# Optimization experiments

Hardware: AMD Instinct MI355X
Metric: run time of the kernel (lower is better)

Reference implementation:

```python
import jax, jax.numpy as jnp
import numpy as np

D = 1024      # d_model
ED = 2048     # d_inner
K = 4         # d_conv
N = 16        # d_state
R = 64        # dt_rank
E = 8         # num_experts
TOPK = 2      # num_experts_per_tok
FF = 2048     # mlp_size
EPS = 1e-6
B, L = 1, 2048


def setup_inputs() -> dict:
    key = jax.random.key(0)
    ks = jax.random.split(key, 12)
    def nrm(k, shape, scale=0.02):
        return jax.random.normal(k, shape, jnp.float32) * scale
    return {
        "x": jax.random.normal(ks[0], (B, L, D), jnp.float32),
        "rms1_w": jnp.ones((D,), jnp.float32),
        "rms2_w": jnp.ones((D,), jnp.float32),
        "W_in": nrm(ks[1], (2 * ED, D)),
        "conv_w": nrm(ks[2], (ED, 1, K), 0.1),
        "conv_b": jnp.zeros((ED,), jnp.float32),
        "W_xproj": nrm(ks[3], (R + 2 * N, ED)),
        "W_dt": nrm(ks[4], (ED, R), 0.1),
        "b_dt": jnp.full((ED,), -4.6, jnp.float32),  # softplus(-4.6) ~ 0.01 init dt
        "A_log": jnp.log(jnp.tile(jnp.arange(1, N + 1, dtype=jnp.float32), (ED, 1))),  # S4D-real init
        "D_skip": jnp.ones((ED,), jnp.float32),
        "W_out": nrm(ks[5], (D, ED)),
        "W_router": nrm(ks[6], (E, D)),
        "gate_w": nrm(ks[7], (E, FF, D)),
        "up_w": nrm(ks[8], (E, FF, D)),
        "down_w": nrm(ks[9], (E, D, FF)),
    }


def rmsnorm(x, w):
    return x * jax.lax.rsqrt(jnp.mean(x * x, -1, keepdims=True) + EPS) * w


def mamba(x, W_in, conv_w, conv_b, W_xproj, W_dt, b_dt, A_log, D_skip, W_out):
    Bb, Ll, _ = x.shape
    xm, z = jnp.split(x @ W_in.T, 2, axis=-1)                 # [B,L,ED] each
    # depthwise causal conv over time
    xc = jax.lax.conv_general_dilated(xm.transpose(0, 2, 1), conv_w, (1,), [(K - 1, 0)],
                                      feature_group_count=ED)  # [B,ED,L]
    xc = jax.nn.silu((xc + conv_b[None, :, None]).transpose(0, 2, 1))  # [B,L,ED]
    dt, Bm, Cm = jnp.split(xc @ W_xproj.T, [R, R + N], axis=-1)        # [B,L,R],[B,L,N],[B,L,N]
    delta = jax.nn.softplus(dt @ W_dt.T + b_dt)                        # [B,L,ED]
    A = -jnp.exp(A_log)                                                # [ED,N]
    dA = jnp.exp(delta[..., None] * A)                                 # [B,L,ED,N]
    dBx = delta[..., None] * Bm[:, :, None, :] * xc[..., None]         # [B,L,ED,N]

    def step(h, t):
        dA_t, dBx_t, C_t = t
        h = dA_t * h + dBx_t
        return h, jnp.einsum("ben,bn->be", h, C_t)

    h0 = jnp.zeros((Bb, ED, N), x.dtype)
    _, ys = jax.lax.scan(step, h0, (dA.transpose(1, 0, 2, 3), dBx.transpose(1, 0, 2, 3), Cm.transpose(1, 0, 2)))
    y = ys.transpose(1, 0, 2) + D_skip * xc
    y = y * jax.nn.silu(z)
    return y @ W_out.T


def moe(x2d, W_router, gate_w, up_w, down_w):
    logits = x2d @ W_router.T                                  # [T,E]
    probs = jax.nn.softmax(logits.astype(jnp.float32), -1)
    topw, sel = jax.lax.top_k(probs, TOPK)                     # NOTE: no renormalization (faithful)
    topw = topw.astype(x2d.dtype)
    wmat = jnp.sum(jax.nn.one_hot(sel, E, dtype=x2d.dtype) * topw[..., None], axis=1)  # [T,E]
    g = jnp.einsum("td,efd->tef", x2d, gate_w)
    u = jnp.einsum("td,efd->tef", x2d, up_w)
    h = jax.nn.silu(g) * u
    ye = jnp.einsum("tef,edf->ted", h, down_w)
    out = jnp.einsum("ted,te->td", ye, wmat)
    return out, logits


def reference(x, rms1_w, rms2_w, W_in, conv_w, conv_b, W_xproj, W_dt, b_dt, A_log,
              D_skip, W_out, W_router, gate_w, up_w, down_w):
    Bb, Ll, Dd = x.shape
    res = x
    h = rmsnorm(x, rms1_w)
    h = mamba(h, W_in, conv_w, conv_b, W_xproj, W_dt, b_dt, A_log, D_skip, W_out)
    x = res + h
    res = x
    h = rmsnorm(x, rms2_w)
    mo, logits = moe(h.reshape(-1, Dd), W_router, gate_w, up_w, down_w)
    x = res + mo.reshape(Bb, Ll, Dd)
    return (x, logits)
```

## Files before the change

kernel.cpp:

```cpp
#include <hip/hip_runtime.h>
#include <math.h>

typedef unsigned short u16;
typedef unsigned int   u32;
typedef __attribute__((ext_vector_type(8))) short bf16x8;
typedef __attribute__((ext_vector_type(4))) float f32x4;

constexpr int Tn=2048, Dm=1024, EDc=2048, Ns=16, Rr=64, NEx=8, FFc=2048;
constexpr int SCH=32, SNCH=Tn/SCH;
constexpr int MAXTM=40;
constexpr float LOG2E = 1.44269504f;

__device__ __forceinline__ float siluf(float x){ return __fdividef(x, 1.f + __expf(-x)); }
__device__ __forceinline__ u16 bfr(float f){
  u32 u = __float_as_uint(f);
  return (u16)((u + 0x7fffu + ((u>>16)&1u)) >> 16);
}
__device__ __forceinline__ float b2f(u16 h){ return __uint_as_float(((u32)h)<<16); }

__device__ __forceinline__ void gload16(const void* g, void* l){
  __builtin_amdgcn_global_load_lds((const __attribute__((address_space(1))) void*)g,
                                   (__attribute__((address_space(3))) void*)l, 16, 0, 0);
}

__global__ __launch_bounds__(256) void f2b_k(const float* __restrict__ in,
                                             u16* __restrict__ out, int n4){
  int i = blockIdx.x*256 + threadIdx.x;
  if (i >= n4) return;
  float4 v = ((const float4*)in)[i];
  u32 lo = (u32)bfr(v.x) | ((u32)bfr(v.y)<<16);
  u32 hi = (u32)bfr(v.z) | ((u32)bfr(v.w)<<16);
  ((uint2*)out)[i] = make_uint2(lo, hi);
}

__global__ __launch_bounds__(256) void f2b3_k(
    const float* __restrict__ g, const float* __restrict__ u,
    const float* __restrict__ d,
    u16* __restrict__ og, u16* __restrict__ ou, u16* __restrict__ od){
  const int BPW = (NEx*FFc*Dm/4)/256;
  int b = blockIdx.x;
  int which = b / BPW;
  int i = (b - which*BPW)*256 + threadIdx.x;
  const float* in = (which==0) ? g : (which==1) ? u : d;
  u16* out        = (which==0) ? og : (which==1) ? ou : od;
  float4 v = ((const float4*)in)[i];
  u32 lo = (u32)bfr(v.x) | ((u32)bfr(v.y)<<16);
  u32 hi = (u32)bfr(v.z) | ((u32)bfr(v.w)<<16);
  ((uint2*)out)[i] = make_uint2(lo, hi);
}

__global__ __launch_bounds__(256) void rmsnorm_k(const float* __restrict__ x,
                                                 const float* __restrict__ w,
                                                 u16* __restrict__ ob){
  int t = blockIdx.x;
  const float* xr = x + (size_t)t * Dm;
  float v[4]; float s = 0.f;
#pragma unroll
  for (int j = 0; j < 4; j++){ int d = threadIdx.x + j*256; v[j] = xr[d]; s += v[j]*v[j]; }
#pragma unroll
  for (int m = 1; m < 64; m <<= 1) s += __shfl_xor(s, m);
  __shared__ float red[4]; __shared__ float sb;
  int lane = threadIdx.x & 63, wv = threadIdx.x >> 6;
  if (lane == 0) red[wv] = s;
  __syncthreads();
  if (threadIdx.x == 0) sb = rsqrtf((red[0]+red[1]+red[2]+red[3]) * (1.f/Dm) + 1e-6f);
  __syncthreads();
  float sc = sb;
#pragma unroll
  for (int j = 0; j < 4; j++){
    int d = threadIdx.x + j*256;
    ob[(size_t)t*Dm + d] = bfr(v[j]*sc*w[d]);
  }
}

__global__ __launch_bounds__(256) void rms2red_k(
  const float* __restrict__ x, const float* __restrict__ P,
  const float* __restrict__ w,
  float* __restrict__ out, float* __restrict__ h2f, u16* __restrict__ h2b)
{
  int t = blockIdx.x, tid = threadIdx.x;
  const size_t S = (size_t)Tn*Dm;
  float v[4]; float s = 0.f;
#pragma unroll
  for (int j = 0; j < 4; j++){
    int d = tid + j*256;
    size_t idx = (size_t)t*Dm + d;
    float a = x[idx] + ((P[idx] + P[S+idx]) + (P[2*S+idx] + P[3*S+idx]));
    out[idx] = a; v[j] = a; s += a*a;
  }
#pragma unroll
  for (int m = 1; m < 64; m <<= 1) s += __shfl_xor(s, m);
  __shared__ float red[4]; __shared__ float sb;
  int lane = tid & 63, wv = tid >> 6;
  if (lane == 0) red[wv] = s;
  __syncthreads();
  if (tid == 0) sb = rsqrtf((red[0]+red[1]+red[2]+red[3]) * (1.f/Dm) + 1e-6f);
  __syncthreads();
  float sc = sb;
#pragma unroll
  for (int j = 0; j < 4; j++){
    int d = tid + j*256;
    float o = v[j]*sc*w[d];
    h2b[(size_t)t*Dm + d] = bfr(o);
    h2f[(size_t)t*Dm + d] = o;
  }
}

template<int EPI, int OB>
__global__ __launch_bounds__(512) void gemm_bb(
    const u16* __restrict__ A, int lda,
    const u16* __restrict__ B, int ldb,
    void* __restrict__ Cv, int ldc,
    int M, int N, int Ksl, const float* __restrict__ aux)
{
  __shared__ u16 As[2*4096], Bs[2*4096];
  int tid = threadIdx.x, lane = tid & 63, wid = tid >> 6;
  int wr = wid >> 2, wc = wid & 3;
  int n0 = blockIdx.x * 128, m0 = blockIdx.y * 128;
  int r = tid >> 2;
  int kk = ((tid & 3) ^ (r & 3)) * 8;
  size_t kbeg = (size_t)blockIdx.z * Ksl;
  const u16* Ag = A + (size_t)min(m0 + r, M-1)*lda + kbeg + kk;
  const u16* Bg = B + (size_t)min(n0 + r, N-1)*ldb + kbeg + kk;
  f32x4 acc[4][2] = {};
  int sw = ((lane>>4) ^ (lane&3)) * 8;
  int aoff[4], boff[2];
#pragma unroll
  for (int i = 0; i < 4; i++) aoff[i] = (wr*64 + i*16 + (lane&15))*32 + sw;
#pragma unroll
  for (int j = 0; j < 2; j++) boff[j] = (wc*32 + j*16 + (lane&15))*32 + sw;
  gload16(Ag, As + tid*8);
  gload16(Bg, Bs + tid*8);
  int NT = Ksl >> 5;
  for (int kt = 0; kt < NT; kt++){
    int cur = (kt & 1) * 4096;
    if (kt + 1 < NT){
      int nxt = 4096 - cur;
      gload16(Ag + (size_t)(kt+1)*32, As + nxt + tid*8);
      gload16(Bg + (size_t)(kt+1)*32, Bs + nxt + tid*8);
      asm volatile("s_waitcnt vmcnt(2)" ::: "memory");
    } else {
      asm volatile("s_waitcnt vmcnt(0)" ::: "memory");
    }
    __builtin_amdgcn_s_barrier();
    bf16x8 af[4], bv[2];
#pragma unroll
    for (int i = 0; i < 4; i++) af[i] = *(const bf16x8*)&As[cur + aoff[i]];
#pragma unroll
    for (int j = 0; j < 2; j++) bv[j] = *(const bf16x8*)&Bs[cur + boff[j]];
    asm volatile("s_waitcnt lgkmcnt(0)" ::: "memory");
    __builtin_amdgcn_sched_barrier(0);
    __builtin_amdgcn_s_barrier();
    __builtin_amdgcn_s_setprio(1);
#pragma unroll
    for (int i = 0; i < 4; i++)
#pragma unroll
      for (int j = 0; j < 2; j++)
        acc[i][j] = __builtin_amdgcn_mfma_f32_16x16x32_bf16(af[i], bv[j], acc[i][j], 0,0,0);
    __builtin_amdgcn_s_setprio(0);
  }
  float* Cf = (float*)Cv + (size_t)blockIdx.z * M * ldc;
  u16*   Cb = (u16*)Cv;
#pragma unroll
  for (int i = 0; i < 4; i++){
    int rbase = m0 + wr*64 + i*16 + ((lane>>4)<<2);
#pragma unroll
    for (int j = 0; j < 2; j++){
      int col = n0 + wc*32 + j*16 + (lane&15);
      if (col >= N) continue;
#pragma unroll
      for (int q = 0; q < 4; q++){
        int row = rbase + q;
        if (row >= M) continue;
        float v = acc[i][j][q];
        if (EPI == 1){ v += aux[col]; v = (v > 20.f) ? v : __logf(1.f + __expf(v)); }
        if (OB) Cb[(size_t)row*ldc + col] = bfr(v);
        else    Cf[(size_t)row*ldc + col] = v;
      }
    }
  }
}

__global__ __launch_bounds__(512) void gateup8(
    const u16* __restrict__ Aall,
    const u16* __restrict__ Wg, const u16* __restrict__ Wu,
    const int* __restrict__ cnt, const int* __restrict__ off,
    const int* __restrict__ bucket,
    const int* __restrict__ tmap, const int* __restrict__ ntot,
    u16* __restrict__ H)
{
  if ((int)blockIdx.y >= *ntot) return;
  int v = tmap[blockIdx.y];
  int e = v >> 16, m0 = (v & 0xFFFF) * 128;
  int Me = cnt[e];
  __shared__ u16 As[2*4096], Gs[2*4096], Us[2*4096];
  int tid = threadIdx.x, lane = tid & 63, wid = tid >> 6;
  int wr = wid >> 2, wc = wid & 3;
  int n0 = blockIdx.x * 128;
  int r = tid >> 2;
  int kk = ((tid & 3) ^ (r & 3)) * 8;
  int arow = bucket[e*Tn + min(m0 + r, Me-1)];
  const u16* Ag = Aall + (size_t)arow*Dm + kk;
  const u16* Gg = Wg + ((size_t)e*FFc + n0 + r)*Dm + kk;
  const u16* Ug = Wu + ((size_t)e*FFc + n0 + r)*Dm + kk;
  f32x4 ag[4][2] = {}, au[4][2] = {};
  int sw = ((lane>>4) ^ (lane&3)) * 8;
  int aoff[4], boff[2];
#pragma unroll
  for (int i = 0; i < 4; i++) aoff[i] = (wr*64 + i*16 + (lane&15))*32 + sw;
#pragma unroll
  for (int j = 0; j < 2; j++) boff[j] = (wc*32 + j*16 + (lane&15))*32 + sw;
  gload16(Ag, As + tid*8);
  gload16(Gg, Gs + tid*8);
  gload16(Ug, Us + tid*8);
  const int NT = Dm >> 5;
  for (int kt = 0; kt < NT; kt++){
    int cur = (kt & 1) * 4096;
    if (kt + 1 < NT){
      int nxt = 4096 - cur;
      gload16(Ag + (size_t)(kt+1)*32, As + nxt + tid*8);
      gload16(Gg + (size_t)(kt+1)*32, Gs + nxt + tid*8);
      gload16(Ug + (size_t)(kt+1)*32, Us + nxt + tid*8);
      asm volatile("s_waitcnt vmcnt(3)" ::: "memory");
    } else {
      asm volatile("s_waitcnt vmcnt(0)" ::: "memory");
    }
    __builtin_amdgcn_s_barrier();
    bf16x8 af[4], gf[2], uf[2];
#pragma unroll
    for (int i = 0; i < 4; i++) af[i] = *(const bf16x8*)&As[cur + aoff[i]];
#pragma unroll
    for (int j = 0; j < 2; j++){ gf[j] = *(const bf16x8*)&Gs[cur + boff[j]];
                                 uf[j] = *(const bf16x8*)&Us[cur + boff[j]]; }
    asm volatile("s_waitcnt lgkmcnt(0)" ::: "memory");
    __builtin_amdgcn_sched_barrier(0);
    __builtin_amdgcn_s_barrier();
    __builtin_amdgcn_s_setprio(1);
#pragma unroll
    for (int i = 0; i < 4; i++)
#pragma unroll
      for (int j = 0; j < 2; j++){
        ag[i][j] = __builtin_amdgcn_mfma_f32_16x16x32_bf16(af[i], gf[j], ag[i][j], 0,0,0);
        au[i][j] = __builtin_amdgcn_mfma_f32_16x16x32_bf16(af[i], uf[j], au[i][j], 0,0,0);
      }
    __builtin_amdgcn_s_setprio(0);
  }
  int offe = off[e];
#pragma unroll
  for (int i = 0; i < 4; i++){
    int mb = m0 + wr*64 + i*16 + ((lane>>4)<<2);
#pragma unroll
    for (int j = 0; j < 2; j++){
      int col = n0 + wc*32 + j*16 + (lane&15);
#pragma unroll
      for (int q = 0; q < 4; q++){
        int m = mb + q;
        if (m >= Me) continue;
        float g = ag[i][j][q], u = au[i][j][q];
        H[(size_t)(offe + m)*FFc + col] = bfr(siluf(g)*u);
      }
    }
  }
}

__global__ __launch_bounds__(512) void down8(
    const u16* __restrict__ Hall, const u16* __restrict__ Wd,
    const int* __restrict__ cnt, const int* __restrict__ off,
    const int* __restrict__ tmap, const int* __restrict__ ntot,
    u16* __restrict__ Y)
{
  if ((int)blockIdx.y >= *ntot) return;
  int v = tmap[blockIdx.y];
  int e = v >> 16, m0 = (v & 0xFFFF) * 128;
  int Me = cnt[e];
  int offe = off[e];
  int kbeg = blockIdx.z * (FFc/2);
  const u16* A = Hall + (size_t)offe*FFc;
  const u16* B = Wd + (size_t)e*Dm*FFc;
  u16* C = Y + (size_t)blockIdx.z*(2*Tn)*Dm + (size_t)offe*Dm;
  __shared__ u16 As[2*4096], Bs[2*4096];
  int tid = threadIdx.x, lane = tid & 63, wid = tid >> 6;
  int wr = wid >> 2, wc = wid & 3;
  int n0 = blockIdx.x * 128;
  int r = tid >> 2;
  int kk = ((tid & 3) ^ (r & 3)) * 8;
  const u16* Ag = A + (size_t)min(m0 + r, Me-1)*FFc + kbeg + kk;
  const u16* Bg = B + (size_t)(n0 + r)*FFc + kbeg + kk;
  f32x4 acc[4][2] = {};
  int sw = ((lane>>4) ^ (lane&3)) * 8;
  int aoff[4], boff[2];
#pragma unroll
  for (int i = 0; i < 4; i++) aoff[i] = (wr*64 + i*16 + (lane&15))*32 + sw;
#pragma unroll
  for (int j = 0; j < 2; j++) boff[j] = (wc*32 + j*16 + (lane&15))*32 + sw;
  gload16(Ag, As + tid*8);
  gload16(Bg, Bs + tid*8);
  const int NT = (FFc/2) >> 5;
  for (int kt = 0; kt < NT; kt++){
    int cur = (kt & 1) * 4096;
    if (kt + 1 < NT){
      int nxt = 4096 - cur;
      gload16(Ag + (size_t)(kt+1)*32, As + nxt + tid*8);
      gload16(Bg + (size_t)(kt+1)*32, Bs + nxt + tid*8);
      asm volatile("s_waitcnt vmcnt(2)" ::: "memory");
    } else {
      asm volatile("s_waitcnt vmcnt(0)" ::: "memory");
    }
    __builtin_amdgcn_s_barrier();
    bf16x8 af[4], bv[2];
#pragma unroll
    for (int i = 0; i < 4; i++) af[i] = *(const bf16x8*)&As[cur + aoff[i]];
#pragma unroll
    for (int j = 0; j < 2; j++) bv[j] = *(const bf16x8*)&Bs[cur + boff[j]];
    asm volatile("s_waitcnt lgkmcnt(0)" ::: "memory");
    __builtin_amdgcn_sched_barrier(0);
    __builtin_amdgcn_s_barrier();
    __builtin_amdgcn_s_setprio(1);
#pragma unroll
    for (int i = 0; i < 4; i++)
#pragma unroll
      for (int j = 0; j < 2; j++)
        acc[i][j] = __builtin_amdgcn_mfma_f32_16x16x32_bf16(af[i], bv[j], acc[i][j], 0,0,0);
    __builtin_amdgcn_s_setprio(0);
  }
#pragma unroll
  for (int i = 0; i < 4; i++){
    int mb = m0 + wr*64 + i*16 + ((lane>>4)<<2);
#pragma unroll
    for (int j = 0; j < 2; j++){
      int col = n0 + wc*32 + j*16 + (lane&15);
#pragma unroll
      for (int q = 0; q < 4; q++){
        int m = mb + q;
        if (m >= Me) continue;
        C[(size_t)m*Dm + col] = bfr(acc[i][j][q]);
      }
    }
  }
}

__global__ __launch_bounds__(256) void conv_k(const u16* __restrict__ xzb,
    const float* __restrict__ cw, const float* __restrict__ cb,
    u16* __restrict__ xc)
{
  int idx = blockIdx.x*256 + threadIdx.x;
  int t = idx >> 11, e = idx & (EDc - 1);
  float v = cb[e];
#pragma unroll
  for (int k = 0; k < 4; k++){
    int tt = t - 3 + k;
    if (tt >= 0) v += b2f(xzb[(size_t)tt*(2*EDc) + e]) * cw[e*4 + k];
  }
  xc[(size_t)t*EDc + e] = bfr(siluf(v));
}

__global__ __launch_bounds__(256) void xp_red(const float* __restrict__ part,
                                              float* __restrict__ xp,
                                              u16* __restrict__ dtA){
  int i = blockIdx.x*256 + threadIdx.x;
  const int S = Tn*96;
  float v = part[i] + part[S + i] + part[2*S + i] + part[3*S + i];
  xp[i] = v;
  int t = i / 96, c = i - t*96;
  if (c < Rr) dtA[t*Rr + c] = bfr(v);
}

__global__ __launch_bounds__(256) void scan_p1(
  const u16* __restrict__ delta, const u16* __restrict__ xc,
// ... 164 lines not shown
  __shared__ float lg[8];
  int lane = tid & 63, wv = tid >> 6;
  if (lane == 0)
#pragma unroll
    for (int e = 0; e < 8; e++) part[wv][e] = p[e];
  __syncthreads();
  if (tid < 8){
    float v = part[0][tid]+part[1][tid]+part[2][tid]+part[3][tid];
    lg[tid] = v;
    logits_out[(size_t)t*8 + tid] = v;
  }
  __syncthreads();
  if (tid == 0){
    float mx = lg[0];
#pragma unroll
    for (int e = 1; e < 8; e++) mx = fmaxf(mx, lg[e]);
    float ex[8], s = 0.f;
#pragma unroll
    for (int e = 0; e < 8; e++){ ex[e] = expf(lg[e] - mx); s += ex[e]; }
    float inv = 1.f / s;
    int i0 = 0; float b0 = ex[0]*inv;
#pragma unroll
    for (int e = 1; e < 8; e++){ float pe = ex[e]*inv; if (pe > b0){ b0 = pe; i0 = e; } }
    int i1 = -1; float b1 = -1e30f;
#pragma unroll
    for (int e = 0; e < 8; e++){ if (e == i0) continue; float pe = ex[e]*inv; if (pe > b1){ b1 = pe; i1 = e; } }
    int k0 = atomicAdd(&cnt[i0], 1); bucket[i0*Tn + k0] = t;
    int k1 = atomicAdd(&cnt[i1], 1); bucket[i1*Tn + k1] = t;
    tok_e[2*t] = i0;   tok_idx[2*t] = k0;   tok_w[2*t] = b0;
    tok_e[2*t+1] = i1; tok_idx[2*t+1] = k1; tok_w[2*t+1] = b1;
  }
}

__global__ void prefix_k(const int* __restrict__ cnt, int* __restrict__ off,
                         int* __restrict__ tmap, int* __restrict__ ntot){
  if (threadIdx.x == 0 && blockIdx.x == 0){
    int s = 0;
    for (int e = 0; e < NEx; e++){ off[e] = s; s += cnt[e]; }
    int nt = 0;
    for (int e = 0; e < NEx; e++){
      int tiles = (cnt[e] + 127) >> 7;
      for (int tm = 0; tm < tiles; tm++) tmap[nt++] = (e << 16) | tm;
    }
    *ntot = nt;
  }
}

__global__ __launch_bounds__(256) void combine_k(float* __restrict__ out,
    const u16* __restrict__ Y, const int* __restrict__ off,
    const int* __restrict__ tok_e, const int* __restrict__ tok_idx,
    const float* __restrict__ tok_w)
{
  int t = blockIdx.x, tid = threadIdx.x;
  const size_t S2 = (size_t)(2*Tn)*Dm;
  int e0 = tok_e[2*t],   e1 = tok_e[2*t+1];
  size_t r0 = (size_t)(off[e0] + tok_idx[2*t])*Dm;
  size_t r1 = (size_t)(off[e1] + tok_idx[2*t+1])*Dm;
  float w0 = tok_w[2*t], w1 = tok_w[2*t+1];
#pragma unroll
  for (int j = 0; j < 4; j++){
    int d = tid + j*256;
    float y0 = b2f(Y[r0 + d]) + b2f(Y[S2 + r0 + d]);
    float y1 = b2f(Y[r1 + d]) + b2f(Y[S2 + r1 + d]);
    out[(size_t)t*Dm + d] += w0*y0 + w1*y1;
  }
}

extern "C" void kernel_launch(void* const* d_in, const int* in_sizes, int n_in,
                              void* d_out, int out_size, void* d_ws, size_t ws_size,
                              hipStream_t stream) {
  const float* x      = (const float*)d_in[0];
  const float* rms1_w = (const float*)d_in[1];
  const float* rms2_w = (const float*)d_in[2];
  const float* W_in   = (const float*)d_in[3];
  const float* conv_w = (const float*)d_in[4];
  const float* conv_b = (const float*)d_in[5];
  const float* W_xprj = (const float*)d_in[6];
  const float* W_dt   = (const float*)d_in[7];
  const float* b_dt   = (const float*)d_in[8];
  const float* A_log  = (const float*)d_in[9];
  const float* D_skip = (const float*)d_in[10];
  const float* W_out  = (const float*)d_in[11];
  const float* W_rt   = (const float*)d_in[12];
  const float* gate_w = (const float*)d_in[13];
  const float* up_w   = (const float*)d_in[14];
  const float* down_w = (const float*)d_in[15];

  float* out        = (float*)d_out;
  float* logits_out = out + (size_t)Tn*Dm;

  uint8_t* base = (uint8_t*)d_ws;
  size_t o = 0;
  auto alloc = [&](size_t bytes) -> void* {
    void* p = base + o;
    o = (o + bytes + 255) & ~(size_t)255;
    return p;
  };
  float* h2f   = (float*)alloc((size_t)Tn*Dm*4);
  u16*   h2b   = (u16*)  alloc((size_t)Tn*Dm*2);
  u16*   hmoe  = (u16*)  alloc((size_t)2*Tn*FFc*2);
  u16*   yslot = (u16*)  alloc((size_t)2*(2*Tn)*Dm*2);
  int*   cnt     = (int*)alloc(64);
  int*   off     = (int*)alloc(64);
  int*   ntot    = (int*)alloc(64);
  int*   tmap    = (int*)alloc(MAXTM*4 + 192);
  int*   bucket  = (int*)alloc((size_t)NEx*Tn*4);
  int*   tok_e   = (int*)alloc((size_t)2*Tn*4);
  int*   tok_idx = (int*)alloc((size_t)2*Tn*4);
  float* tok_w   = (float*)alloc((size_t)2*Tn*4);
  size_t oz = o;
  u16*   xzb   = (u16*)  alloc((size_t)Tn*2*EDc*2);
  u16*   delta = (u16*)  alloc((size_t)Tn*EDc*2);
  u16*   xc    = (u16*)  alloc((size_t)Tn*EDc*2);
  u16*   y2    = (u16*)  alloc((size_t)Tn*EDc*2);
  u16*   h1b   = (u16*)  alloc((size_t)Tn*Dm*2);
  u16*   dtA   = (u16*)  alloc((size_t)Tn*Rr*2);
  float* xp    = (float*)alloc((size_t)Tn*96*4);
  float* xp_part=(float*)alloc((size_t)4*Tn*96*4);
  float* hend  = (float*)alloc((size_t)SNCH*EDc*Ns*4);
  float* hin   = (float*)alloc((size_t)SNCH*EDc*Ns*4);
  float* dsum  = (float*)alloc((size_t)SNCH*EDc*4);
  float* wpart = (float*)xzb;
  u16* wgate = (u16*)(base + oz);
  u16* wup   = wgate + (size_t)NEx*FFc*Dm;
  u16* wdown = wup   + (size_t)NEx*FFc*Dm;
  u16* wbin  = (u16*)yslot;
  u16* wbout = wbin + (size_t)2*EDc*Dm;
  u16* wxp   = (u16*)hmoe;
  u16* wdt   = wxp + (size_t)96*EDc;

  f2b_k<<<(2*EDc*Dm/4)/256, 256, 0, stream>>>(W_in,   wbin,  2*EDc*Dm/4);
  f2b_k<<<(Dm*EDc/4)/256,   256, 0, stream>>>(W_out,  wbout, Dm*EDc/4);
  f2b_k<<<(96*EDc/4)/256,   256, 0, stream>>>(W_xprj, wxp,   96*EDc/4);
  f2b_k<<<(EDc*Rr/4)/256,   256, 0, stream>>>(W_dt,   wdt,   EDc*Rr/4);
  rmsnorm_k<<<Tn, 256, 0, stream>>>(x, rms1_w, h1b);
  gemm_bb<0,1><<<dim3(32,16,1), 512, 0, stream>>>(h1b, Dm, wbin, Dm, xzb, 2*EDc, Tn, 2*EDc, Dm, nullptr);
  conv_k<<<(Tn*EDc)/256, 256, 0, stream>>>(xzb, conv_w, conv_b, xc);
  gemm_bb<0,0><<<dim3(1,16,4), 512, 0, stream>>>(xc, EDc, wxp, EDc, xp_part, 96, Tn, 96, EDc/4, nullptr);
  xp_red<<<(Tn*96)/256, 256, 0, stream>>>(xp_part, xp, dtA);
  gemm_bb<1,1><<<dim3(16,16,1), 512, 0, stream>>>(dtA, Rr, wdt, Rr, delta, EDc, Tn, EDc, Rr, b_dt);
  scan_p1<<<dim3(EDc/256, SNCH), 256, 0, stream>>>(delta, xc, xp, A_log, hend, dsum);
  scan_p2<<<EDc*Ns/256, 256, 0, stream>>>(hend, dsum, A_log, hin);
  scan_p3<<<dim3(EDc/256, SNCH), 256, 0, stream>>>(delta, xc, xp, xzb, A_log, D_skip, hin, y2);
  gemm_bb<0,0><<<dim3(8,16,4), 512, 0, stream>>>(y2, EDc, wbout, EDc, wpart, Dm, Tn, Dm, EDc/4, nullptr);
  rms2red_k<<<Tn, 256, 0, stream>>>(x, wpart, rms2_w, out, h2f, h2b);
  f2b3_k<<<3*((NEx*FFc*Dm/4)/256), 256, 0, stream>>>(gate_w, up_w, down_w, wgate, wup, wdown);
  hipMemsetAsync(cnt, 0, 32, stream);
  route_k<<<Tn, 256, 0, stream>>>(h2f, W_rt, logits_out, cnt, bucket, tok_e, tok_idx, tok_w);
  prefix_k<<<1, 64, 0, stream>>>(cnt, off, tmap, ntot);
  gateup8<<<dim3(16, MAXTM), 512, 0, stream>>>(h2b, wgate, wup, cnt, off, bucket, tmap, ntot, hmoe);
  down8<<<dim3(8, MAXTM, 2), 512, 0, stream>>>(hmoe, wdown, cnt, off, tmap, ntot, yslot);
  combine_k<<<Tn, 256, 0, stream>>>(out, yslot, off, tok_e, tok_idx, tok_w);
}
```

Baseline: 395.7 us.

## Fuse fp32-to-bf16 weight conversion into GEMM and MoE B-operand loads

Removes the separate passes that convert W_in, W_out and the expert gate, up and down weights to bf16. The GEMM and MoE kernels now read fp32 weights straight into registers, pack them with v_cvt_pk_bf16_f32 and store them to LDS, with the next tile's loads issued before the current MFMAs. This saves a full write and re-read of about 200MB of expert weights. In exchange the MoE GEMMs read twice as many weight bytes, repeated per token tile, and lose the async direct-to-LDS load path for B. The gate and up MFMA phases are also split so the up-weight LDS reads are issued separately.

```diff
diff --git a/kernel.cpp b/kernel.cpp
--- a/kernel.cpp
+++ b/kernel.cpp
@@ -17,6 +17,13 @@
   return (u16)((u + 0x7fffu + ((u>>16)&1u)) >> 16);
 }
 __device__ __forceinline__ float b2f(u16 h){ return __uint_as_float(((u32)h)<<16); }
+
+__device__ __forceinline__ u32 cvtpk(float lo, float hi){
+  u32 r; asm("v_cvt_pk_bf16_f32 %0, %1, %2" : "=v"(r) : "v"(lo), "v"(hi)); return r;
+}
+__device__ __forceinline__ uint4 cvt8(float4 a, float4 b){
+  return make_uint4(cvtpk(a.x,a.y), cvtpk(a.z,a.w), cvtpk(b.x,b.y), cvtpk(b.z,b.w));
+}
 
 __device__ __forceinline__ void gload16(const void* g, void* l){
   __builtin_amdgcn_global_load_lds((const __attribute__((address_space(1))) void*)g,
@@ -33,22 +40,6 @@
   ((uint2*)out)[i] = make_uint2(lo, hi);
 }
 
-__global__ __launch_bounds__(256) void f2b3_k(
-    const float* __restrict__ g, const float* __restrict__ u,
-    const float* __restrict__ d,
-    u16* __restrict__ og, u16* __restrict__ ou, u16* __restrict__ od){
-  const int BPW = (NEx*FFc*Dm/4)/256;
-  int b = blockIdx.x;
-  int which = b / BPW;
-  int i = (b - which*BPW)*256 + threadIdx.x;
-  const float* in = (which==0) ? g : (which==1) ? u : d;
-  u16* out        = (which==0) ? og : (which==1) ? ou : od;
-  float4 v = ((const float4*)in)[i];
-  u32 lo = (u32)bfr(v.x) | ((u32)bfr(v.y)<<16);
-  u32 hi = (u32)bfr(v.z) | ((u32)bfr(v.w)<<16);
-  ((uint2*)out)[i] = make_uint2(lo, hi);
-}
-
 __global__ __launch_bounds__(256) void rmsnorm_k(const float* __restrict__ x,
                                                  const float* __restrict__ w,
                                                  u16* __restrict__ ob){
@@ -106,10 +97,10 @@
   }
 }
 
-template<int EPI, int OB>
+template<int EPI, int OB, int BF32>
 __global__ __launch_bounds__(512) void gemm_bb(
     const u16* __restrict__ A, int lda,
-    const u16* __restrict__ B, int ldb,
+    const void* __restrict__ Bvp, int ldb,
     void* __restrict__ Cv, int ldc,
     int M, int N, int Ksl, const float* __restrict__ aux)
 {
@@ -121,7 +112,6 @@
   int kk = ((tid & 3) ^ (r & 3)) * 8;
   size_t kbeg = (size_t)blockIdx.z * Ksl;
   const u16* Ag = A + (size_t)min(m0 + r, M-1)*lda + kbeg + kk;
-  const u16* Bg = B + (size_t)min(n0 + r, N-1)*ldb + kbeg + kk;
   f32x4 acc[4][2] = {};
   int sw = ((lane>>4) ^ (lane&3)) * 8;
   int aoff[4], boff[2];
@@ -129,36 +119,81 @@
   for (int i = 0; i < 4; i++) aoff[i] = (wr*64 + i*16 + (lane&15))*32 + sw;
 #pragma unroll
   for (int j = 0; j < 2; j++) boff[j] = (wc*32 + j*16 + (lane&15))*32 + sw;
-  gload16(Ag, As + tid*8);
-  gload16(Bg, Bs + tid*8);
   int NT = Ksl >> 5;
-  for (int kt = 0; kt < NT; kt++){
-    int cur = (kt & 1) * 4096;
-    if (kt + 1 < NT){
-      int nxt = 4096 - cur;
-      gload16(Ag + (size_t)(kt+1)*32, As + nxt + tid*8);
-      gload16(Bg + (size_t)(kt+1)*32, Bs + nxt + tid*8);
-      asm volatile("s_waitcnt vmcnt(2)" ::: "memory");
-    } else {
+
+  if (BF32){
+    const float* Bg = (const float*)Bvp + (size_t)min(n0 + r, N-1)*ldb + kbeg + kk;
+    {
+      float4 q0 = *(const float4*)Bg;
+      float4 q1 = *(const float4*)(Bg + 4);
+      gload16(Ag, As + tid*8);
       asm volatile("s_waitcnt vmcnt(0)" ::: "memory");
-    }
-    __builtin_amdgcn_s_barrier();
-    bf16x8 af[4], bv[2];
-#pragma unroll
-    for (int i = 0; i < 4; i++) af[i] = *(const bf16x8*)&As[cur + aoff[i]];
-#pragma unroll
-    for (int j = 0; j < 2; j++) bv[j] = *(const bf16x8*)&Bs[cur + boff[j]];
-    asm volatile("s_waitcnt lgkmcnt(0)" ::: "memory");
-    __builtin_amdgcn_sched_barrier(0);
-    __builtin_amdgcn_s_barrier();
-    __builtin_amdgcn_s_setprio(1);
-#pragma unroll
-    for (int i = 0; i < 4; i++)
-#pragma unroll
-      for (int j = 0; j < 2; j++)
-        acc[i][j] = __builtin_amdgcn_mfma_f32_16x16x32_bf16(af[i], bv[j], acc[i][j], 0,0,0);
-    __builtin_amdgcn_s_setprio(0);
-  }
+      *(uint4*)&Bs[tid*8] = cvt8(q0, q1);
+    }
+    for (int kt = 0; kt < NT; kt++){
+      int cur = (kt & 1) * 4096, nxt = 4096 - cur;
+      bool pf = (kt + 1 < NT);
+      float4 p0{}, p1{};
+      if (pf){
+        p0 = *(const float4*)(Bg + (size_t)(kt+1)*32);
+        p1 = *(const float4*)(Bg + (size_t)(kt+1)*32 + 4);
+        gload16(Ag + (size_t)(kt+1)*32, As + nxt + tid*8);
+      }
+      asm volatile("s_waitcnt lgkmcnt(0)" ::: "memory");
+      __builtin_amdgcn_s_barrier();
+      bf16x8 af[4], bv[2];
+#pragma unroll
+      for (int i = 0; i < 4; i++) af[i] = *(const bf16x8*)&As[cur + aoff[i]];
+#pragma unroll
+      for (int j = 0; j < 2; j++) bv[j] = *(const bf16x8*)&Bs[cur + boff[j]];
+      asm volatile("s_waitcnt lgkmcnt(0)" ::: "memory");
+      __builtin_amdgcn_sched_barrier(0);
+      __builtin_amdgcn_s_barrier();
+      __builtin_amdgcn_s_setprio(1);
+#pragma unroll
+      for (int i = 0; i < 4; i++)
+#pragma unroll
+        for (int j = 0; j < 2; j++)
+          acc[i][j] = __builtin_amdgcn_mfma_f32_16x16x32_bf16(af[i], bv[j], acc[i][j], 0,0,0);
+      __builtin_amdgcn_s_setprio(0);
+      if (pf){
+        asm volatile("s_waitcnt vmcnt(0)" ::: "memory");
+        *(uint4*)&Bs[nxt + tid*8] = cvt8(p0, p1);
+      }
+    }
+  } else {
+    const u16* Bg = (const u16*)Bvp + (size_t)min(n0 + r, N-1)*ldb + kbeg + kk;
+    gload16(Ag, As + tid*8);
+    gload16(Bg, Bs + tid*8);
+    for (int kt = 0; kt < NT; kt++){
+      int cur = (kt & 1) * 4096;
+      if (kt + 1 < NT){
+        int nxt = 4096 - cur;
+        gload16(Ag + (size_t)(kt+1)*32, As + nxt + tid*8);
+        gload16(Bg + (size_t)(kt+1)*32, Bs + nxt + tid*8);
+        asm volatile("s_waitcnt vmcnt(2)" ::: "memory");
+      } else {
+        asm volatile("s_waitcnt vmcnt(0)" ::: "memory");
+      }
+      __builtin_amdgcn_s_barrier();
+      bf16x8 af[4], bv[2];
+#pragma unroll
+      for (int i = 0; i < 4; i++) af[i] = *(const bf16x8*)&As[cur + aoff[i]];
+#pragma unroll
+      for (int j = 0; j < 2; j++) bv[j] = *(const bf16x8*)&Bs[cur + boff[j]];
+      asm volatile("s_waitcnt lgkmcnt(0)" ::: "memory");
+      __builtin_amdgcn_sched_barrier(0);
+      __builtin_amdgcn_s_barrier();
+      __builtin_amdgcn_s_setprio(1);
+#pragma unroll
+      for (int i = 0; i < 4; i++)
+#pragma unroll
+        for (int j = 0; j < 2; j++)
+          acc[i][j] = __builtin_amdgcn_mfma_f32_16x16x32_bf16(af[i], bv[j], acc[i][j], 0,0,0);
+      __builtin_amdgcn_s_setprio(0);
+    }
+  }
+
   float* Cf = (float*)Cv + (size_t)blockIdx.z * M * ldc;
   u16*   Cb = (u16*)Cv;
 #pragma unroll
@@ -183,7 +218,7 @@
 
 __global__ __launch_bounds__(512) void gateup8(
     const u16* __restrict__ Aall,
-    const u16* __restrict__ Wg, const u16* __restrict__ Wu,
+    const float* __restrict__ Wg, const float* __restrict__ Wu,
     const int* __restrict__ cnt, const int* __restrict__ off,
     const int* __restrict__ bucket,
     const int* __restrict__ tmap, const int* __restrict__ ntot,
@@ -201,8 +236,8 @@
   int kk = ((tid & 3) ^ (r & 3)) * 8;
   int arow = bucket[e*Tn + min(m0 + r, Me-1)];
   const u16* Ag = Aall + (size_t)arow*Dm + kk;
-  const u16* Gg = Wg + ((size_t)e*FFc + n0 + r)*Dm + kk;
-  const u16* Ug = Wu + ((size_t)e*FFc + n0 + r)*Dm + kk;
+  const float* Gg = Wg + ((size_t)e*FFc + n0 + r)*Dm + kk;
+  const float* Ug = Wu + ((size_t)e*FFc + n0 + r)*Dm + kk;
   f32x4 ag[4][2] = {}, au[4][2] = {};
   int sw = ((lane>>4) ^ (lane&3)) * 8;
   int aoff[4], boff[2];
@@ -210,28 +245,33 @@
   for (int i = 0; i < 4; i++) aoff[i] = (wr*64 + i*16 + (lane&15))*32 + sw;
 #pragma unroll
   for (int j = 0; j < 2; j++) boff[j] = (wc*32 + j*16 + (lane&15))*32 + sw;
-  gload16(Ag, As + tid*8);
-  gload16(Gg, Gs + tid*8);
-  gload16(Ug, Us + tid*8);
+  {
+    float4 g0 = *(const float4*)Gg, g1 = *(const float4*)(Gg + 4);
+    float4 u0 = *(const float4*)Ug, u1 = *(const float4*)(Ug + 4);
+    gload16(Ag, As + tid*8);
+    asm volatile("s_waitcnt vmcnt(0)" ::: "memory");
+    *(uint4*)&Gs[tid*8] = cvt8(g0, g1);
+    *(uint4*)&Us[tid*8] = cvt8(u0, u1);
+  }
   const int NT = Dm >> 5;
   for (int kt = 0; kt < NT; kt++){
-    int cur = (kt & 1) * 4096;
-    if (kt + 1 < NT){
-      int nxt = 4096 - cur;
+    int cur = (kt & 1) * 4096, nxt = 4096 - cur;
+    bool pf = (kt + 1 < NT);
+    float4 g0{}, g1{}, u0{}, u1{};
+    if (pf){
+      g0 = *(const float4*)(Gg + (size_t)(kt+1)*32);
+      g1 = *(const float4*)(Gg + (size_t)(kt+1)*32 + 4);
+      u0 = *(const float4*)(Ug + (size_t)(kt+1)*32);
+      u1 = *(const float4*)(Ug + (size_t)(kt+1)*32 + 4);
       gload16(Ag + (size_t)(kt+1)*32, As + nxt + tid*8);
-      gload16(Gg + (size_t)(kt+1)*32, Gs + nxt + tid*8);
-      gload16(Ug + (size_t)(kt+1)*32, Us + nxt + tid*8);
-      asm volatile("s_waitcnt vmcnt(3)" ::: "memory");
-    } else {
-      asm volatile("s_waitcnt vmcnt(0)" ::: "memory");
-    }
+    }
+    asm volatile("s_waitcnt lgkmcnt(0)" ::: "memory");
     __builtin_amdgcn_s_barrier();
     bf16x8 af[4], gf[2], uf[2];
 #pragma unroll
     for (int i = 0; i < 4; i++) af[i] = *(const bf16x8*)&As[cur + aoff[i]];
 #pragma unroll
-    for (int j = 0; j < 2; j++){ gf[j] = *(const bf16x8*)&Gs[cur + boff[j]];
-                                 uf[j] = *(const bf16x8*)&Us[cur + boff[j]]; }
+    for (int j = 0; j < 2; j++) gf[j] = *(const bf16x8*)&Gs[cur + boff[j]];
     asm volatile("s_waitcnt lgkmcnt(0)" ::: "memory");
     __builtin_amdgcn_sched_barrier(0);
     __builtin_amdgcn_s_barrier();
@@ -239,11 +279,23 @@
 #pragma unroll
     for (int i = 0; i < 4; i++)
 #pragma unroll
-      for (int j = 0; j < 2; j++){
+      for (int j = 0; j < 2; j++)
         ag[i][j] = __builtin_amdgcn_mfma_f32_16x16x32_bf16(af[i], gf[j], ag[i][j], 0,0,0);
+#pragma unroll
+    for (int j = 0; j < 2; j++) uf[j] = *(const bf16x8*)&Us[cur + boff[j]];
+    asm volatile("s_waitcnt lgkmcnt(0)" ::: "memory");
+    __builtin_amdgcn_sched_barrier(0);
+#pragma unroll
+    for (int i = 0; i < 4; i++)
+#pragma unroll
+      for (int j = 0; j < 2; j++)
         au[i][j] = __builtin_amdgcn_mfma_f32_16x16x32_bf16(af[i], uf[j], au[i][j], 0,0,0);
-      }
     __builtin_amdgcn_s_setprio(0);
+    if (pf){
+      asm volatile("s_waitcnt vmcnt(0)" ::: "memory");
+      *(uint4*)&Gs[nxt + tid*8] = cvt8(g0, g1);
+      *(uint4*)&Us[nxt + tid*8] = cvt8(u0, u1);
+    }
   }
   int offe = off[e];
 #pragma unroll
@@ -264,7 +316,7 @@
 }
 
 __global__ __launch_bounds__(512) void down8(
-    const u16* __restrict__ Hall, const u16* __restrict__ Wd,
+    const u16* __restrict__ Hall, const float* __restrict__ Wd,
     const int* __restrict__ cnt, const int* __restrict__ off,
     const int* __restrict__ tmap, const int* __restrict__ ntot,
     u16* __restrict__ Y)
@@ -276,7 +328,6 @@
   int offe = off[e];
   int kbeg = blockIdx.z * (FFc/2);
   const u16* A = Hall + (size_t)offe*FFc;
-  const u16* B = Wd + (size_t)e*Dm*FFc;
   u16* C = Y + (size_t)blockIdx.z*(2*Tn)*Dm + (size_t)offe*Dm;
   __shared__ u16 As[2*4096], Bs[2*4096];
   int tid = threadIdx.x, lane = tid & 63, wid = tid >> 6;
@@ -285,7 +336,7 @@
   int r = tid >> 2;
   int kk = ((tid & 3) ^ (r & 3)) * 8;
   const u16* Ag = A + (size_t)min(m0 + r, Me-1)*FFc + kbeg + kk;
-  const u16* Bg = B + (size_t)(n0 + r)*FFc + kbeg + kk;
+  const float* Bg = Wd + (size_t)e*Dm*FFc + (size_t)(n0 + r)*FFc + kbeg + kk;
   f32x4 acc[4][2] = {};
   int sw = ((lane>>4) ^ (lane&3)) * 8;
   int aoff[4], boff[2];
@@ -293,19 +344,23 @@
   for (int i = 0; i < 4; i++) aoff[i] = (wr*64 + i*16 + (lane&15))*32 + sw;
 #pragma unroll
   for (int j = 0; j < 2; j++) boff[j] = (wc*32 + j*16 + (lane&15))*32 + sw;
-  gload16(Ag, As + tid*8);
-  gload16(Bg, Bs + tid*8);
+  {
+    float4 q0 = *(const float4*)Bg, q1 = *(const float4*)(Bg + 4);
+    gload16(Ag, As + tid*8);
+    asm volatile("s_waitcnt vmcnt(0)" ::: "memory");
+    *(uint4*)&Bs[tid*8] = cvt8(q0, q1);
+  }
   const int NT = (FFc/2) >> 5;
   for (int kt = 0; kt < NT; kt++){
-    int cur = (kt & 1) * 4096;
-    if (kt + 1 < NT){
-      int nxt = 4096 - cur;
+    int cur = (kt & 1) * 4096, nxt = 4096 - cur;
+    bool pf = (kt + 1 < NT);
+    float4 p0{}, p1{};
+    if (pf){
+      p0 = *(const float4*)(Bg + (size_t)(kt+1)*32);
+      p1 = *(const float4*)(Bg + (size_t)(kt+1)*32 + 4);
       gload16(Ag + (size_t)(kt+1)*32, As + nxt + tid*8);
-      gload16(Bg + (size_t)(kt+1)*32, Bs + nxt + tid*8);
-      asm volatile("s_waitcnt vmcnt(2)" ::: "memory");
-    } else {
-      asm volatile("s_waitcnt vmcnt(0)" ::: "memory");
-    }
+    }
+    asm volatile("s_waitcnt lgkmcnt(0)" ::: "memory");
     __builtin_amdgcn_s_barrier();
     bf16x8 af[4], bv[2];
 #pragma unroll
@@ -322,6 +377,10 @@
       for (int j = 0; j < 2; j++)
         acc[i][j] = __builtin_amdgcn_mfma_f32_16x16x32_bf16(af[i], bv[j], acc[i][j], 0,0,0);
     __builtin_amdgcn_s_setprio(0);
+    if (pf){
+      asm volatile("s_waitcnt vmcnt(0)" ::: "memory");
+      *(uint4*)&Bs[nxt + tid*8] = cvt8(p0, p1);
+    }
   }
 #pragma unroll
   for (int i = 0; i < 4; i++){
@@ -640,7 +699,6 @@
   int*   tok_e   = (int*)alloc((size_t)2*Tn*4);
   int*   tok_idx = (int*)alloc((size_t)2*Tn*4);
   float* tok_w   = (float*)alloc((size_t)2*Tn*4);
-  size_t oz = o;
   u16*   xzb   = (u16*)  alloc((size_t)Tn*2*EDc*2);
   u16*   delta = (u16*)  alloc((size_t)Tn*EDc*2);
   u16*   xc    = (u16*)  alloc((size_t)Tn*EDc*2);
@@ -653,34 +711,26 @@
   float* hin   = (float*)alloc((size_t)SNCH*EDc*Ns*4);
   float* dsum  = (float*)alloc((size_t)SNCH*EDc*4);
   float* wpart = (float*)xzb;
-  u16* wgate = (u16*)(base + oz);
-  u16* wup   = wgate + (size_t)NEx*FFc*Dm;
-  u16* wdown = wup   + (size_t)NEx*FFc*Dm;
-  u16* wbin  = (u16*)yslot;
-  u16* wbout = wbin + (size_t)2*EDc*Dm;
   u16* wxp   = (u16*)hmoe;
   u16* wdt   = wxp + (size_t)96*EDc;
 
-  f2b_k<<<(2*EDc*Dm/4)/256, 256, 0, stream>>>(W_in,   wbin,  2*EDc*Dm/4);
-  f2b_k<<<(Dm*EDc/4)/256,   256, 0, stream>>>(W_out,  wbout, Dm*EDc/4);
   f2b_k<<<(96*EDc/4)/256,   256, 0, stream>>>(W_xprj, wxp,   96*EDc/4);
   f2b_k<<<(EDc*Rr/4)/256,   256, 0, stream>>>(W_dt,   wdt,   EDc*Rr/4);
   rmsnorm_k<<<Tn, 256, 0, stream>>>(x, rms1_w, h1b);
-  gemm_bb<0,1><<<dim3(32,16,1), 512, 0, stream>>>(h1b, Dm, wbin, Dm, xzb, 2*EDc, Tn, 2*EDc, Dm, nullptr);
+  gemm_bb<0,1,1><<<dim3(32,16,1), 512, 0, stream>>>(h1b, Dm, W_in, Dm, xzb, 2*EDc, Tn, 2*EDc, Dm, nullptr);
   conv_k<<<(Tn*EDc)/256, 256, 0, stream>>>(xzb, conv_w, conv_b, xc);
-  gemm_bb<0,0><<<dim3(1,16,4), 512, 0, stream>>>(xc, EDc, wxp, EDc, xp_part, 96, Tn, 96, EDc/4, nullptr);
+  gemm_bb<0,0,0><<<dim3(1,16,4), 512, 0, stream>>>(xc, EDc, wxp, EDc, xp_part, 96, Tn, 96, EDc/4, nullptr);
   xp_red<<<(Tn*96)/256, 256, 0, stream>>>(xp_part, xp, dtA);
-  gemm_bb<1,1><<<dim3(16,16,1), 512, 0, stream>>>(dtA, Rr, wdt, Rr, delta, EDc, Tn, EDc, Rr, b_dt);
+  gemm_bb<1,1,0><<<dim3(16,16,1), 512, 0, stream>>>(dtA, Rr, wdt, Rr, delta, EDc, Tn, EDc, Rr, b_dt);
   scan_p1<<<dim3(EDc/256, SNCH), 256, 0, stream>>>(delta, xc, xp, A_log, hend, dsum);
   scan_p2<<<EDc*Ns/256, 256, 0, stream>>>(hend, dsum, A_log, hin);
   scan_p3<<<dim3(EDc/256, SNCH), 256, 0, stream>>>(delta, xc, xp, xzb, A_log, D_skip, hin, y2);
-  gemm_bb<0,0><<<dim3(8,16,4), 512, 0, stream>>>(y2, EDc, wbout, EDc, wpart, Dm, Tn, Dm, EDc/4, nullptr);
+  gemm_bb<0,0,1><<<dim3(8,16,4), 512, 0, stream>>>(y2, EDc, W_out, EDc, wpart, Dm, Tn, Dm, EDc/4, nullptr);
   rms2red_k<<<Tn, 256, 0, stream>>>(x, wpart, rms2_w, out, h2f, h2b);
-  f2b3_k<<<3*((NEx*FFc*Dm/4)/256), 256, 0, stream>>>(gate_w, up_w, down_w, wgate, wup, wdown);
   hipMemsetAsync(cnt, 0, 32, stream);
   route_k<<<Tn, 256, 0, stream>>>(h2f, W_rt, logits_out, cnt, bucket, tok_e, tok_idx, tok_w);
   prefix_k<<<1, 64, 0, stream>>>(cnt, off, tmap, ntot);
-  gateup8<<<dim3(16, MAXTM), 512, 0, stream>>>(h2b, wgate, wup, cnt, off, bucket, tmap, ntot, hmoe);
-  down8<<<dim3(8, MAXTM, 2), 512, 0, stream>>>(hmoe, wdown, cnt, off, tmap, ntot, yslot);
+  gateup8<<<dim3(16, MAXTM), 512, 0, stream>>>(h2b, gate_w, up_w, cnt, off, bucket, tmap, ntot, hmoe);
+  down8<<<dim3(8, MAXTM, 2), 512, 0, stream>>>(hmoe, down_w, cnt, off, tmap, ntot, yslot);
   combine_k<<<Tn, 256, 0, stream>>>(out, yslot, off, tok_e, tok_idx, tok_w);
 }
```

Measured after the change: 410.9 us. 1.04x slower.

## Launch one block per expert column tile and loop over M tiles inside

Applied to the files above, without the earlier changes.

Replaces the flattened (expert, M-tile) grid of the MoE gate/up and down kernels with a grid of one block per expert and N-tile, where each block loops over its expert's M tiles. This removes the tile-map construction and the early-exit empty blocks. The weight tile is reloaded for each M tile, but grid parallelism drops from up to 40×16 blocks to 8×16 blocks, so long serial loops on heavily loaded experts risk load imbalance and underuse of the CUs.

```diff
diff --git a/kernel.cpp b/kernel.cpp
--- a/kernel.cpp
+++ b/kernel.cpp
@@ -8,7 +8,6 @@
 
 constexpr int Tn=2048, Dm=1024, EDc=2048, Ns=16, Rr=64, NEx=8, FFc=2048;
 constexpr int SCH=32, SNCH=Tn/SCH;
-constexpr int MAXTM=40;
 constexpr float LOG2E = 1.44269504f;
 
 __device__ __forceinline__ float siluf(float x){ return __fdividef(x, 1.f + __expf(-x)); }
@@ -186,78 +185,79 @@
     const u16* __restrict__ Wg, const u16* __restrict__ Wu,
     const int* __restrict__ cnt, const int* __restrict__ off,
     const int* __restrict__ bucket,
-    const int* __restrict__ tmap, const int* __restrict__ ntot,
     u16* __restrict__ H)
 {
-  if ((int)blockIdx.y >= *ntot) return;
-  int v = tmap[blockIdx.y];
-  int e = v >> 16, m0 = (v & 0xFFFF) * 128;
+  int e = blockIdx.y;
   int Me = cnt[e];
+  int ntile = (Me + 127) >> 7;
   __shared__ u16 As[2*4096], Gs[2*4096], Us[2*4096];
   int tid = threadIdx.x, lane = tid & 63, wid = tid >> 6;
   int wr = wid >> 2, wc = wid & 3;
   int n0 = blockIdx.x * 128;
   int r = tid >> 2;
   int kk = ((tid & 3) ^ (r & 3)) * 8;
-  int arow = bucket[e*Tn + min(m0 + r, Me-1)];
-  const u16* Ag = Aall + (size_t)arow*Dm + kk;
   const u16* Gg = Wg + ((size_t)e*FFc + n0 + r)*Dm + kk;
   const u16* Ug = Wu + ((size_t)e*FFc + n0 + r)*Dm + kk;
-  f32x4 ag[4][2] = {}, au[4][2] = {};
   int sw = ((lane>>4) ^ (lane&3)) * 8;
   int aoff[4], boff[2];
 #pragma unroll
   for (int i = 0; i < 4; i++) aoff[i] = (wr*64 + i*16 + (lane&15))*32 + sw;
 #pragma unroll
   for (int j = 0; j < 2; j++) boff[j] = (wc*32 + j*16 + (lane&15))*32 + sw;
-  gload16(Ag, As + tid*8);
-  gload16(Gg, Gs + tid*8);
-  gload16(Ug, Us + tid*8);
+  int offe = off[e];
   const int NT = Dm >> 5;
-  for (int kt = 0; kt < NT; kt++){
-    int cur = (kt & 1) * 4096;
-    if (kt + 1 < NT){
-      int nxt = 4096 - cur;
-      gload16(Ag + (size_t)(kt+1)*32, As + nxt + tid*8);
-      gload16(Gg + (size_t)(kt+1)*32, Gs + nxt + tid*8);
-      gload16(Ug + (size_t)(kt+1)*32, Us + nxt + tid*8);
-      asm volatile("s_waitcnt vmcnt(3)" ::: "memory");
-    } else {
-      asm volatile("s_waitcnt vmcnt(0)" ::: "memory");
-    }
-    __builtin_amdgcn_s_barrier();
-    bf16x8 af[4], gf[2], uf[2];
-#pragma unroll
-    for (int i = 0; i < 4; i++) af[i] = *(const bf16x8*)&As[cur + aoff[i]];
-#pragma unroll
-    for (int j = 0; j < 2; j++){ gf[j] = *(const bf16x8*)&Gs[cur + boff[j]];
-                                 uf[j] = *(const bf16x8*)&Us[cur + boff[j]]; }
-    asm volatile("s_waitcnt lgkmcnt(0)" ::: "memory");
-    __builtin_amdgcn_sched_barrier(0);
-    __builtin_amdgcn_s_barrier();
-    __builtin_amdgcn_s_setprio(1);
-#pragma unroll
-    for (int i = 0; i < 4; i++)
+  for (int mt = 0; mt < ntile; mt++){
+    int m0 = mt * 128;
+    int arow = bucket[e*Tn + min(m0 + r, Me-1)];
+    const u16* Ag = Aall + (size_t)arow*Dm + kk;
+    f32x4 ag[4][2] = {}, au[4][2] = {};
+    gload16(Ag, As + tid*8);
+    gload16(Gg, Gs + tid*8);
+    gload16(Ug, Us + tid*8);
+    for (int kt = 0; kt < NT; kt++){
+      int cur = (kt & 1) * 4096;
+      if (kt + 1 < NT){
+        int nxt = 4096 - cur;
+        gload16(Ag + (size_t)(kt+1)*32, As + nxt + tid*8);
+        gload16(Gg + (size_t)(kt+1)*32, Gs + nxt + tid*8);
+        gload16(Ug + (size_t)(kt+1)*32, Us + nxt + tid*8);
+        asm volatile("s_waitcnt vmcnt(3)" ::: "memory");
+      } else {
+        asm volatile("s_waitcnt vmcnt(0)" ::: "memory");
+      }
+      __builtin_amdgcn_s_barrier();
+      bf16x8 af[4], gf[2], uf[2];
+#pragma unroll
+      for (int i = 0; i < 4; i++) af[i] = *(const bf16x8*)&As[cur + aoff[i]];
+#pragma unroll
+      for (int j = 0; j < 2; j++){ gf[j] = *(const bf16x8*)&Gs[cur + boff[j]];
+                                   uf[j] = *(const bf16x8*)&Us[cur + boff[j]]; }
+      asm volatile("s_waitcnt lgkmcnt(0)" ::: "memory");
+      __builtin_amdgcn_sched_barrier(0);
+      __builtin_amdgcn_s_barrier();
+      __builtin_amdgcn_s_setprio(1);
+#pragma unroll
+      for (int i = 0; i < 4; i++)
+#pragma unroll
+        for (int j = 0; j < 2; j++){
+          ag[i][j] = __builtin_amdgcn_mfma_f32_16x16x32_bf16(af[i], gf[j], ag[i][j], 0,0,0);
+          au[i][j] = __builtin_amdgcn_mfma_f32_16x16x32_bf16(af[i], uf[j], au[i][j], 0,0,0);
+        }
+      __builtin_amdgcn_s_setprio(0);
+    }
+#pragma unroll
+    for (int i = 0; i < 4; i++){
+      int mb = m0 + wr*64 + i*16 + ((lane>>4)<<2);
 #pragma unroll
       for (int j = 0; j < 2; j++){
-        ag[i][j] = __builtin_amdgcn_mfma_f32_16x16x32_bf16(af[i], gf[j], ag[i][j], 0,0,0);
-        au[i][j] = __builtin_amdgcn_mfma_f32_16x16x32_bf16(af[i], uf[j], au[i][j], 0,0,0);
-      }
-    __builtin_amdgcn_s_setprio(0);
-  }
-  int offe = off[e];
-#pragma unroll
-  for (int i = 0; i < 4; i++){
-    int mb = m0 + wr*64 + i*16 + ((lane>>4)<<2);
-#pragma unroll
-    for (int j = 0; j < 2; j++){
-      int col = n0 + wc*32 + j*16 + (lane&15);
-#pragma unroll
-      for (int q = 0; q < 4; q++){
-        int m = mb + q;
-        if (m >= Me) continue;
-        float g = ag[i][j][q], u = au[i][j][q];
-        H[(size_t)(offe + m)*FFc + col] = bfr(siluf(g)*u);
+        int col = n0 + wc*32 + j*16 + (lane&15);
+#pragma unroll
+        for (int q = 0; q < 4; q++){
+          int m = mb + q;
+          if (m >= Me) continue;
+          float g = ag[i][j][q], u = au[i][j][q];
+          H[(size_t)(offe + m)*FFc + col] = bfr(siluf(g)*u);
+        }
       }
     }
   }
@@ -266,17 +266,14 @@
 __global__ __launch_bounds__(512) void down8(
     const u16* __restrict__ Hall, const u16* __restrict__ Wd,
     const int* __restrict__ cnt, const int* __restrict__ off,
-    const int* __restrict__ tmap, const int* __restrict__ ntot,
     u16* __restrict__ Y)
 {
-  if ((int)blockIdx.y >= *ntot) return;
-  int v = tmap[blockIdx.y];
-  int e = v >> 16, m0 = (v & 0xFFFF) * 128;
+  int e = blockIdx.y;
   int Me = cnt[e];
+  int ntile = (Me + 127) >> 7;
   int offe = off[e];
   int kbeg = blockIdx.z * (FFc/2);
   const u16* A = Hall + (size_t)offe*FFc;
-  const u16* B = Wd + (size_t)e*Dm*FFc;
   u16* C = Y + (size_t)blockIdx.z*(2*Tn)*Dm + (size_t)offe*Dm;
   __shared__ u16 As[2*4096], Bs[2*4096];
   int tid = threadIdx.x, lane = tid & 63, wid = tid >> 6;
@@ -284,56 +281,59 @@
   int n0 = blockIdx.x * 128;
   int r = tid >> 2;
   int kk = ((tid & 3) ^ (r & 3)) * 8;
-  const u16* Ag = A + (size_t)min(m0 + r, Me-1)*FFc + kbeg + kk;
-  const u16* Bg = B + (size_t)(n0 + r)*FFc + kbeg + kk;
-  f32x4 acc[4][2] = {};
+  const u16* Bg = Wd + (size_t)e*Dm*FFc + (size_t)(n0 + r)*FFc + kbeg + kk;
   int sw = ((lane>>4) ^ (lane&3)) * 8;
   int aoff[4], boff[2];
 #pragma unroll
   for (int i = 0; i < 4; i++) aoff[i] = (wr*64 + i*16 + (lane&15))*32 + sw;
 #pragma unroll
   for (int j = 0; j < 2; j++) boff[j] = (wc*32 + j*16 + (lane&15))*32 + sw;
-  gload16(Ag, As + tid*8);
-  gload16(Bg, Bs + tid*8);
   const int NT = (FFc/2) >> 5;
-  for (int kt = 0; kt < NT; kt++){
-    int cur = (kt & 1) * 4096;
-    if (kt + 1 < NT){
-      int nxt = 4096 - cur;
-      gload16(Ag + (size_t)(kt+1)*32, As + nxt + tid*8);
-      gload16(Bg + (size_t)(kt+1)*32, Bs + nxt + tid*8);
-      asm volatile("s_waitcnt vmcnt(2)" ::: "memory");
-    } else {
-      asm volatile("s_waitcnt vmcnt(0)" ::: "memory");
-    }
-    __builtin_amdgcn_s_barrier();
-    bf16x8 af[4], bv[2];
-#pragma unroll
-    for (int i = 0; i < 4; i++) af[i] = *(const bf16x8*)&As[cur + aoff[i]];
-#pragma unroll
-    for (int j = 0; j < 2; j++) bv[j] = *(const bf16x8*)&Bs[cur + boff[j]];
-    asm volatile("s_waitcnt lgkmcnt(0)" ::: "memory");
-    __builtin_amdgcn_sched_barrier(0);
-    __builtin_amdgcn_s_barrier();
-    __builtin_amdgcn_s_setprio(1);
-#pragma unroll
-    for (int i = 0; i < 4; i++)
-#pragma unroll
-      for (int j = 0; j < 2; j++)
-        acc[i][j] = __builtin_amdgcn_mfma_f32_16x16x32_bf16(af[i], bv[j], acc[i][j], 0,0,0);
-    __builtin_amdgcn_s_setprio(0);
-  }
-#pragma unroll
-  for (int i = 0; i < 4; i++){
-    int mb = m0 + wr*64 + i*16 + ((lane>>4)<<2);
-#pragma unroll
-    for (int j = 0; j < 2; j++){
-      int col = n0 + wc*32 + j*16 + (lane&15);
-#pragma unroll
-      for (int q = 0; q < 4; q++){
-        int m = mb + q;
-        if (m >= Me) continue;
-        C[(size_t)m*Dm + col] = bfr(acc[i][j][q]);
+  for (int mt = 0; mt < ntile; mt++){
+    int m0 = mt * 128;
+    const u16* Ag = A + (size_t)min(m0 + r, Me-1)*FFc + kbeg + kk;
+    f32x4 acc[4][2] = {};
+    gload16(Ag, As + tid*8);
+    gload16(Bg, Bs + tid*8);
+    for (int kt = 0; kt < NT; kt++){
+      int cur = (kt & 1) * 4096;
+      if (kt + 1 < NT){
+        int nxt = 4096 - cur;
+        gload16(Ag + (size_t)(kt+1)*32, As + nxt + tid*8);
+        gload16(Bg + (size_t)(kt+1)*32, Bs + nxt + tid*8);
+        asm volatile("s_waitcnt vmcnt(2)" ::: "memory");
+      } else {
+        asm volatile("s_waitcnt vmcnt(0)" ::: "memory");
+      }
+      __builtin_amdgcn_s_barrier();
+      bf16x8 af[4], bv[2];
+#pragma unroll
+      for (int i = 0; i < 4; i++) af[i] = *(const bf16x8*)&As[cur + aoff[i]];
+#pragma unroll
+      for (int j = 0; j < 2; j++) bv[j] = *(const bf16x8*)&Bs[cur + boff[j]];
+      asm volatile("s_waitcnt lgkmcnt(0)" ::: "memory");
+      __builtin_amdgcn_sched_barrier(0);
+      __builtin_amdgcn_s_barrier();
+      __builtin_amdgcn_s_setprio(1);
+#pragma unroll
+      for (int i = 0; i < 4; i++)
+#pragma unroll
+        for (int j = 0; j < 2; j++)
+          acc[i][j] = __builtin_amdgcn_mfma_f32_16x16x32_bf16(af[i], bv[j], acc[i][j], 0,0,0);
+      __builtin_amdgcn_s_setprio(0);
+    }
+#pragma unroll
+    for (int i = 0; i < 4; i++){
+      int mb = m0 + wr*64 + i*16 + ((lane>>4)<<2);
+#pragma unroll
+      for (int j = 0; j < 2; j++){
+        int col = n0 + wc*32 + j*16 + (lane&15);
+#pragma unroll
+        for (int q = 0; q < 4; q++){
+          int m = mb + q;
+          if (m >= Me) continue;
+          C[(size_t)m*Dm + col] = bfr(acc[i][j][q]);
+        }
       }
     }
   }
@@ -564,17 +564,10 @@
   }
 }
 
-__global__ void prefix_k(const int* __restrict__ cnt, int* __restrict__ off,
-                         int* __restrict__ tmap, int* __restrict__ ntot){
+__global__ void prefix_k(const int* __restrict__ cnt, int* __restrict__ off){
   if (threadIdx.x == 0 && blockIdx.x == 0){
     int s = 0;
     for (int e = 0; e < NEx; e++){ off[e] = s; s += cnt[e]; }
-    int nt = 0;
-    for (int e = 0; e < NEx; e++){
-      int tiles = (cnt[e] + 127) >> 7;
-      for (int tm = 0; tm < tiles; tm++) tmap[nt++] = (e << 16) | tm;
-    }
-    *ntot = nt;
   }
 }
 
@@ -634,8 +627,6 @@
   u16*   yslot = (u16*)  alloc((size_t)2*(2*Tn)*Dm*2);
   int*   cnt     = (int*)alloc(64);
   int*   off     = (int*)alloc(64);
-  int*   ntot    = (int*)alloc(64);
-  int*   tmap    = (int*)alloc(MAXTM*4 + 192);
   int*   bucket  = (int*)alloc((size_t)NEx*Tn*4);
   int*   tok_e   = (int*)alloc((size_t)2*Tn*4);
   int*   tok_idx = (int*)alloc((size_t)2*Tn*4);
@@ -679,8 +670,8 @@
   f2b3_k<<<3*((NEx*FFc*Dm/4)/256), 256, 0, stream>>>(gate_w, up_w, down_w, wgate, wup, wdown);
   hipMemsetAsync(cnt, 0, 32, stream);
   route_k<<<Tn, 256, 0, stream>>>(h2f, W_rt, logits_out, cnt, bucket, tok_e, tok_idx, tok_w);
-  prefix_k<<<1, 64, 0, stream>>>(cnt, off, tmap, ntot);
-  gateup8<<<dim3(16, MAXTM), 512, 0, stream>>>(h2b, wgate, wup, cnt, off, bucket, tmap, ntot, hmoe);
-  down8<<<dim3(8, MAXTM, 2), 512, 0, stream>>>(hmoe, wdown, cnt, off, tmap, ntot, yslot);
+  prefix_k<<<1, 64, 0, stream>>>(cnt, off);
+  gateup8<<<dim3(16, NEx), 512, 0, stream>>>(h2b, wgate, wup, cnt, off, bucket, hmoe);
+  down8<<<dim3(8, NEx, 2), 512, 0, stream>>>(hmoe, wdown, cnt, off, yslot);
   combine_k<<<Tn, 256, 0, stream>>>(out, yslot, off, tok_e, tok_idx, tok_w);
 }
```

After: 530.0 us. +34.0%, slower.
